# Kernel tuning notes

Measured on AMD Instinct MI355X. Metric: run time of the kernel, lower is better.

The kernel has to match this reference:

```python
import jax, jax.numpy as jnp
import numpy as np

B, N, D_IN, D_HID, D_EDGE = 4, 256, 256, 256, 64


def setup_inputs() -> dict:
    key = jax.random.key(0)
    ks = jax.random.split(key, 8)
    s_in = 1.0 / np.sqrt(D_IN)
    s_h2 = 1.0 / np.sqrt(2 * D_HID)
    s_h = 1.0 / np.sqrt(D_HID)
    return {
        "x": jax.random.normal(ks[0], (B, N, D_IN), jnp.float32),
        "W_in": jax.random.uniform(ks[1], (D_HID, D_IN), jnp.float32, -s_in, s_in),
        "b_in": jax.random.uniform(ks[2], (D_HID,), jnp.float32, -s_in, s_in),
        "W1": jax.random.uniform(ks[3], (D_HID, 2 * D_HID), jnp.float32, -s_h2, s_h2),
        "b1": jax.random.uniform(ks[4], (D_HID,), jnp.float32, -s_h2, s_h2),
        "W2": jax.random.uniform(ks[5], (D_EDGE, D_HID), jnp.float32, -s_h, s_h),
        "b2": jax.random.uniform(ks[6], (D_EDGE,), jnp.float32, -s_h, s_h),
    }


def reference(x, W_in, b_in, W1, b1, W2, b2):
    # in_proj: [B,N,d_in] -> [B,N,h]
    h = jnp.einsum("bnd,hd->bnh", x, W_in) + b_in
    # cat([h_i, h_j]) @ W1 == h_i @ Wa + h_j @ Wb with W1 = [Wa | Wb].
    # Precompute the two N x h projections, then broadcast-add over the pair grid
    # instead of materializing the [B,N,N,2h] concat (same math, fused form).
    Wa, Wb = W1[:, :D_HID], W1[:, D_HID:]
    pa = jnp.einsum("bnh,gh->bng", h, Wa)  # [B,N,h]
    pb = jnp.einsum("bnh,gh->bng", h, Wb)  # [B,N,h]
    z = pa[:, :, None, :] + pb[:, None, :, :] + b1  # [B,N,N,h]
    z = z * jax.nn.sigmoid(z)  # Swish
    return jnp.einsum("bijh,eh->bije", z, W2) + b2  # [B,N,N,d_edge]
```

## Files before the change

kernel.cpp:

```cpp
#include <hip/hip_runtime.h>

#define DIN 256
#define DHID 256
#define DEDGE 64
#define GS 68
#define W2_PAD 264

typedef float f32x4 __attribute__((ext_vector_type(4)));
typedef short s16x8 __attribute__((ext_vector_type(8)));
typedef unsigned int u32x4 __attribute__((ext_vector_type(4)));

__device__ __forceinline__ unsigned short f2bf(float f) {
    unsigned int u = __builtin_bit_cast(unsigned int, f);
    u += 0x7fffu + ((u >> 16) & 1u);
    return (unsigned short)(u >> 16);
}
__device__ __forceinline__ unsigned int pk_bf16(float a, float b) {
    return (unsigned int)f2bf(a) | ((unsigned int)f2bf(b) << 16);
}

__global__ __launch_bounds__(256) void k_xh(
    const float* __restrict__ x, const float* __restrict__ Win,
    float* __restrict__ hp)
{
    __shared__ float as[64 * GS];
    __shared__ float ws[64 * GS];
    const int m0 = blockIdx.x << 6, n0 = blockIdx.y << 6, k0 = blockIdx.z << 6;
    const int tid = threadIdx.x;
    const int rr = tid >> 4;
    const int kk = (tid & 15) << 2;

#pragma unroll
    for (int it = 0; it < 4; ++it) {
        const int row = rr + (it << 4);
        *reinterpret_cast<f32x4*>(&as[row * GS + kk]) =
            *reinterpret_cast<const f32x4*>(&x[(m0 + row) * DIN + k0 + kk]);
        *reinterpret_cast<f32x4*>(&ws[row * GS + kk]) =
            *reinterpret_cast<const f32x4*>(&Win[(n0 + row) * DIN + k0 + kk]);
    }
    __syncthreads();

    const int tx = tid & 15, ty = tid >> 4;
    float acc[4][4] = {};
    for (int k = 0; k < 64; k += 4) {
        f32x4 av[4], wv[4];
#pragma unroll
        for (int r = 0; r < 4; ++r)
            av[r] = *reinterpret_cast<const f32x4*>(&as[(ty + (r << 4)) * GS + k]);
#pragma unroll
        for (int c = 0; c < 4; ++c)
            wv[c] = *reinterpret_cast<const f32x4*>(&ws[(tx + (c << 4)) * GS + k]);
#pragma unroll
        for (int r = 0; r < 4; ++r)
#pragma unroll
            for (int c = 0; c < 4; ++c)
                acc[r][c] += av[r][0]*wv[c][0] + av[r][1]*wv[c][1]
                           + av[r][2]*wv[c][2] + av[r][3]*wv[c][3];
    }
    float* dst = hp + ((size_t)blockIdx.z << 18);
#pragma unroll
    for (int r = 0; r < 4; ++r)
#pragma unroll
        for (int c = 0; c < 4; ++c)
            dst[(m0 + ty + (r << 4)) * DHID + n0 + tx + (c << 4)] = acc[r][c];
}

__global__ __launch_bounds__(256) void k_pab(
    const float* __restrict__ hp, const float* __restrict__ W1,
    const float* __restrict__ bin, float* __restrict__ pap, float* __restrict__ pbp)
{
    __shared__ float as[64 * GS];
    __shared__ float ws[64 * GS];
    const int m0 = blockIdx.x << 6;
    const int half = blockIdx.y >> 2;
    const int n0 = (blockIdx.y & 3) << 6;
    const int kc = blockIdx.z;
    const int tid = threadIdx.x;
    const int rr = tid >> 4, kk = (tid & 15) << 2;
    const int tx = tid & 15, ty = tid >> 4;

    float acc[4][4] = {};
    for (int kt = 0; kt < 2; ++kt) {
        const int k0 = (kc << 7) + (kt << 6);
        if (kt) __syncthreads();
#pragma unroll
        for (int it = 0; it < 4; ++it) {
            const int row = rr + (it << 4);
            const int aoff = (m0 + row) * DHID + k0 + kk;
            f32x4 av = *reinterpret_cast<const f32x4*>(&hp[aoff]);
            av += *reinterpret_cast<const f32x4*>(&hp[aoff + (1 << 18)]);
            av += *reinterpret_cast<const f32x4*>(&hp[aoff + (2 << 18)]);
            av += *reinterpret_cast<const f32x4*>(&hp[aoff + (3 << 18)]);
            av += *reinterpret_cast<const f32x4*>(&bin[k0 + kk]);
            *reinterpret_cast<f32x4*>(&as[row * GS + kk]) = av;
            *reinterpret_cast<f32x4*>(&ws[row * GS + kk]) =
                *reinterpret_cast<const f32x4*>(&W1[(n0 + row) * 512 + (half << 8) + k0 + kk]);
        }
        __syncthreads();

        for (int k = 0; k < 64; k += 4) {
            f32x4 av[4], wv[4];
#pragma unroll
            for (int r = 0; r < 4; ++r)
                av[r] = *reinterpret_cast<const f32x4*>(&as[(ty + (r << 4)) * GS + k]);
#pragma unroll
            for (int c = 0; c < 4; ++c)
                wv[c] = *reinterpret_cast<const f32x4*>(&ws[(tx + (c << 4)) * GS + k]);
#pragma unroll
            for (int r = 0; r < 4; ++r)
#pragma unroll
                for (int c = 0; c < 4; ++c)
                    acc[r][c] += av[r][0]*wv[c][0] + av[r][1]*wv[c][1]
                               + av[r][2]*wv[c][2] + av[r][3]*wv[c][3];
        }
    }
    float* dst = (half ? pbp : pap) + ((size_t)kc << 18);
#pragma unroll
    for (int r = 0; r < 4; ++r)
#pragma unroll
        for (int c = 0; c < 4; ++c)
            dst[(m0 + ty + (r << 4)) * DHID + n0 + tx + (c << 4)] = acc[r][c];
}

__global__ __launch_bounds__(256) void k_out(
    const float* __restrict__ pap, const float* __restrict__ pbp,
    const float* __restrict__ b1, const float* __restrict__ W2,
    const float* __restrict__ b2, float* __restrict__ out)
{
    __shared__ unsigned short w2s[DEDGE * W2_PAD];
    __shared__ float pab1[4][DHID];

    const int jb = blockIdx.x, i0 = blockIdx.y << 2, b = blockIdx.z;
    const int tid = threadIdx.x;

    {
        const float b1v = b1[tid];
#pragma unroll
        for (int ii = 0; ii < 4; ++ii) {
            const int off = (((b << 8) + i0 + ii) << 8) + tid;
            pab1[ii][tid] = pap[off] + pap[off + (1 << 18)] + b1v;
        }
    }
#pragma unroll
    for (int it = 0; it < 8; ++it) {
        const int t = tid + (it << 8);
        const int row = t >> 5;
        const int cc = (t & 31) << 3;
        const f32x4 w0 = *reinterpret_cast<const f32x4*>(&W2[row * DHID + cc]);
        const f32x4 w1 = *reinterpret_cast<const f32x4*>(&W2[row * DHID + cc + 4]);
        u32x4 wp;
        wp[0] = pk_bf16(w0[0], w0[1]); wp[1] = pk_bf16(w0[2], w0[3]);
        wp[2] = pk_bf16(w1[0], w1[1]); wp[3] = pk_bf16(w1[2], w1[3]);
        *reinterpret_cast<u32x4*>(&w2s[row * W2_PAD + cc]) = wp;
    }
    __syncthreads();

    const int lane = tid & 63, wave = tid >> 6, quad = lane >> 4, l15 = lane & 15;
    const int j0 = (jb << 6) + (wave << 4);
    const int pboff = (((b << 8) + (j0 + l15)) << 8);
    const float* pbq0 = pbp + pboff;
    const float* pbq1 = pbp + (1 << 18) + pboff;

    f32x4 acc[4][4];
#pragma unroll
    for (int ii = 0; ii < 4; ++ii)
#pragma unroll
        for (int eb = 0; eb < 4; ++eb) acc[ii][eb] = (f32x4){0.f, 0.f, 0.f, 0.f};

    float b2v[4];
#pragma unroll
    for (int eb = 0; eb < 4; ++eb) b2v[eb] = b2[(eb << 4) + l15];

    for (int k0 = 0; k0 < 8; ++k0) {
        const int g = (k0 << 5) + (quad << 3);
        const f32x4 p0 = *reinterpret_cast<const f32x4*>(pbq0 + g)
                       + *reinterpret_cast<const f32x4*>(pbq1 + g);
        const f32x4 p1 = *reinterpret_cast<const f32x4*>(pbq0 + g + 4)
                       + *reinterpret_cast<const f32x4*>(pbq1 + g + 4);

        s16x8 bfrag[4];
#pragma unroll
        for (int eb = 0; eb < 4; ++eb)
            bfrag[eb] = *reinterpret_cast<const s16x8*>(&w2s[((eb << 4) + l15) * W2_PAD + g]);

#pragma unroll
        for (int ii = 0; ii < 4; ++ii) {
            const f32x4 q0 = *reinterpret_cast<const f32x4*>(&pab1[ii][g]);
            const f32x4 q1 = *reinterpret_cast<const f32x4*>(&pab1[ii][g + 4]);
            float s[8];
#pragma unroll
            for (int jj = 0; jj < 4; ++jj) {
                const float z0 = q0[jj] + p0[jj];
                const float z1 = q1[jj] + p1[jj];
                const float e0 = __expf(-z0);
                const float e1 = __expf(-z1);
                s[jj]     = z0 * __builtin_amdgcn_rcpf(1.0f + e0);
                s[4 + jj] = z1 * __builtin_amdgcn_rcpf(1.0f + e1);
            }
            u32x4 ap;
            ap[0] = pk_bf16(s[0], s[1]); ap[1] = pk_bf16(s[2], s[3]);
            ap[2] = pk_bf16(s[4], s[5]); ap[3] = pk_bf16(s[6], s[7]);
            const s16x8 a = __builtin_bit_cast(s16x8, ap);
#pragma unroll
            for (int eb = 0; eb < 4; ++eb)
                acc[ii][eb] = __builtin_amdgcn_mfma_f32_16x16x32_bf16(a, bfrag[eb], acc[ii][eb], 0, 0, 0);
        }
    }

#pragma unroll
    for (int ii = 0; ii < 4; ++ii) {
        const int obase = (((((b << 8) + i0 + ii) << 8) + j0 + (quad << 2)) << 6) + l15;
#pragma unroll
        for (int eb = 0; eb < 4; ++eb) {
#pragma unroll
            for (int r = 0; r < 4; ++r)
                out[obase + (r << 6) + (eb << 4)] = acc[ii][eb][r] + b2v[eb];
        }
    }
}

extern "C" void kernel_launch(void* const* d_in, const int* in_sizes, int n_in,
                              void* d_out, int out_size, void* d_ws, size_t ws_size,
                              hipStream_t stream) {
    const float* x = 0; const float* Win = 0; const float* bin = 0;
    const float* W1 = 0; const float* b1 = 0; const float* W2 = 0; const float* b2 = 0;
    for (int idx = 0; idx < n_in; ++idx) {
        const int s = in_sizes[idx];
        if (s == 262144) x = (const float*)d_in[idx];
        else if (s == 131072) W1 = (const float*)d_in[idx];
        else if (s == 65536) Win = (const float*)d_in[idx];
        else if (s == 16384) W2 = (const float*)d_in[idx];
        else if (s == 64) b2 = (const float*)d_in[idx];
        else if (s == 256) { if (!bin) bin = (const float*)d_in[idx]; else b1 = (const float*)d_in[idx]; }
    }

    float* ws = (float*)d_ws;
    float* hp  = ws;
    float* pap = hp + (4 << 18);
    float* pbp = pap + (2 << 18);

    hipLaunchKernelGGL(k_xh,  dim3(16, 4, 4), dim3(256), 0, stream, x, Win, hp);
    hipLaunchKernelGGL(k_pab, dim3(16, 8, 2), dim3(256), 0, stream, hp, W1, bin, pap, pbp);
    hipLaunchKernelGGL(k_out, dim3(4, 64, 4), dim3(256), 0, stream, pap, pbp, b1, W2, b2, (float*)d_out);
}
```

Baseline: 130.3 us.

## Pre-convert W2 to bf16 MFMA fragment layout once; use hardware bf16 pack and nontemporal stores

W2 is now converted to bf16 once, in extra blocks of the first kernel, and written in the exact per-lane MFMA fragment order. Each k_out block then does a straight 16-byte copy into shared memory and reads fragments by lane index, with no per-block fp32-to-bf16 conversion or padded strided layout. The software round-to-nearest bf16 packing is replaced by the v_cvt_pk_bf16_f32 instruction. Output writes use nontemporal stores to reduce cache pollution. This needs extra workspace, and the blocks that handle the conversion idle most of their threads.

```diff
diff --git a/kernel.cpp b/kernel.cpp
--- a/kernel.cpp
+++ b/kernel.cpp
@@ -4,29 +4,41 @@
 #define DHID 256
 #define DEDGE 64
 #define GS 68
-#define W2_PAD 264
 
 typedef float f32x4 __attribute__((ext_vector_type(4)));
 typedef short s16x8 __attribute__((ext_vector_type(8)));
 typedef unsigned int u32x4 __attribute__((ext_vector_type(4)));
 
-__device__ __forceinline__ unsigned short f2bf(float f) {
-    unsigned int u = __builtin_bit_cast(unsigned int, f);
-    u += 0x7fffu + ((u >> 16) & 1u);
-    return (unsigned short)(u >> 16);
-}
-__device__ __forceinline__ unsigned int pk_bf16(float a, float b) {
-    return (unsigned int)f2bf(a) | ((unsigned int)f2bf(b) << 16);
+__device__ __forceinline__ unsigned int cvtpk(float lo, float hi) {
+    unsigned int r;
+    asm("v_cvt_pk_bf16_f32 %0, %1, %2" : "=v"(r) : "v"(lo), "v"(hi));
+    return r;
 }
 
 __global__ __launch_bounds__(256) void k_xh(
     const float* __restrict__ x, const float* __restrict__ Win,
-    float* __restrict__ hp)
+    float* __restrict__ hp, const float* __restrict__ W2, s16x8* __restrict__ W2f)
 {
+    const int tid = threadIdx.x;
+    if (blockIdx.z == 4) {
+        if (tid < 32) {
+            const int f = (((blockIdx.x << 2) + blockIdx.y) << 5) + tid;
+            const int l15f = f & 15, qf = (f >> 4) & 3, ebf = (f >> 6) & 3, k0f = f >> 8;
+            const int row = (ebf << 4) + l15f;
+            const int col = (k0f << 5) + (qf << 3);
+            const f32x4 w0 = *reinterpret_cast<const f32x4*>(&W2[row * DHID + col]);
+            const f32x4 w1 = *reinterpret_cast<const f32x4*>(&W2[row * DHID + col + 4]);
+            u32x4 wp;
+            wp[0] = cvtpk(w0[0], w0[1]); wp[1] = cvtpk(w0[2], w0[3]);
+            wp[2] = cvtpk(w1[0], w1[1]); wp[3] = cvtpk(w1[2], w1[3]);
+            W2f[f] = __builtin_bit_cast(s16x8, wp);
+        }
+        return;
+    }
+
     __shared__ float as[64 * GS];
     __shared__ float ws[64 * GS];
     const int m0 = blockIdx.x << 6, n0 = blockIdx.y << 6, k0 = blockIdx.z << 6;
-    const int tid = threadIdx.x;
     const int rr = tid >> 4;
     const int kk = (tid & 15) << 2;
 
@@ -124,10 +136,10 @@
 
 __global__ __launch_bounds__(256) void k_out(
     const float* __restrict__ pap, const float* __restrict__ pbp,
-    const float* __restrict__ b1, const float* __restrict__ W2,
+    const float* __restrict__ b1, const s16x8* __restrict__ W2f,
     const float* __restrict__ b2, float* __restrict__ out)
 {
-    __shared__ unsigned short w2s[DEDGE * W2_PAD];
+    __shared__ s16x8 w2s[2048];
     __shared__ float pab1[4][DHID];
 
     const int jb = blockIdx.x, i0 = blockIdx.y << 2, b = blockIdx.z;
@@ -142,17 +154,8 @@
         }
     }
 #pragma unroll
-    for (int it = 0; it < 8; ++it) {
-        const int t = tid + (it << 8);
-        const int row = t >> 5;
-        const int cc = (t & 31) << 3;
-        const f32x4 w0 = *reinterpret_cast<const f32x4*>(&W2[row * DHID + cc]);
-        const f32x4 w1 = *reinterpret_cast<const f32x4*>(&W2[row * DHID + cc + 4]);
-        u32x4 wp;
-        wp[0] = pk_bf16(w0[0], w0[1]); wp[1] = pk_bf16(w0[2], w0[3]);
-        wp[2] = pk_bf16(w1[0], w1[1]); wp[3] = pk_bf16(w1[2], w1[3]);
-        *reinterpret_cast<u32x4*>(&w2s[row * W2_PAD + cc]) = wp;
-    }
+    for (int it = 0; it < 8; ++it)
+        w2s[tid + (it << 8)] = W2f[tid + (it << 8)];
     __syncthreads();
 
     const int lane = tid & 63, wave = tid >> 6, quad = lane >> 4, l15 = lane & 15;
@@ -181,7 +184,7 @@
         s16x8 bfrag[4];
 #pragma unroll
         for (int eb = 0; eb < 4; ++eb)
-            bfrag[eb] = *reinterpret_cast<const s16x8*>(&w2s[((eb << 4) + l15) * W2_PAD + g]);
+            bfrag[eb] = w2s[((k0 << 2) + eb) * 64 + lane];
 
 #pragma unroll
         for (int ii = 0; ii < 4; ++ii) {
@@ -198,8 +201,8 @@
                 s[4 + jj] = z1 * __builtin_amdgcn_rcpf(1.0f + e1);
             }
             u32x4 ap;
-            ap[0] = pk_bf16(s[0], s[1]); ap[1] = pk_bf16(s[2], s[3]);
-            ap[2] = pk_bf16(s[4], s[5]); ap[3] = pk_bf16(s[6], s[7]);
+            ap[0] = cvtpk(s[0], s[1]); ap[1] = cvtpk(s[2], s[3]);
+            ap[2] = cvtpk(s[4], s[5]); ap[3] = cvtpk(s[6], s[7]);
             const s16x8 a = __builtin_bit_cast(s16x8, ap);
 #pragma unroll
             for (int eb = 0; eb < 4; ++eb)
@@ -214,7 +217,8 @@
         for (int eb = 0; eb < 4; ++eb) {
 #pragma unroll
             for (int r = 0; r < 4; ++r)
-                out[obase + (r << 6) + (eb << 4)] = acc[ii][eb][r] + b2v[eb];
+                __builtin_nontemporal_store(acc[ii][eb][r] + b2v[eb],
+                                            &out[obase + (r << 6) + (eb << 4)]);
         }
     }
 }
@@ -234,12 +238,14 @@
         else if (s == 256) { if (!bin) bin = (const float*)d_in[idx]; else b1 = (const float*)d_in[idx]; }
     }
 
-    float* ws = (float*)d_ws;
+    float* ws  = (float*)d_ws;
     float* hp  = ws;
     float* pap = hp + (4 << 18);
     float* pbp = pap + (2 << 18);
-
-    hipLaunchKernelGGL(k_xh,  dim3(16, 4, 4), dim3(256), 0, stream, x, Win, hp);
+    float* w2f = pbp + (2 << 18);
+
+    hipLaunchKernelGGL(k_xh,  dim3(16, 4, 5), dim3(256), 0, stream, x, Win, hp, W2, (s16x8*)w2f);
     hipLaunchKernelGGL(k_pab, dim3(16, 8, 2), dim3(256), 0, stream, hp, W1, bin, pap, pbp);
-    hipLaunchKernelGGL(k_out, dim3(4, 64, 4), dim3(256), 0, stream, pap, pbp, b1, W2, b2, (float*)d_out);
-}
+    hipLaunchKernelGGL(k_out, dim3(4, 64, 4), dim3(256), 0, stream,
+                       pap, pbp, b1, (const s16x8*)w2f, b2, (float*)d_out);
+}
```

After: 125.8 us. 1.04x faster.
